# Optimization experiments

Measured on AMD Instinct MI355X. Metric: run time of the kernel, lower is better.

## Reference

```python
import jax, jax.numpy as jnp
import numpy as np

BIT = 8
Q_MAX = float(2 ** BIT - 1)  # 255
SMOOTH = 0.999


def hardsigmoid(x):
    # torch nn.Hardsigmoid: relu6(x + 3) / 6
    return jnp.clip(x / 6.0 + 0.5, 0.0, 1.0)


def setup_inputs() -> dict:
    key = jax.random.key(0)
    ks = jax.random.split(key, 5)
    B, C, H, W = 64, 256, 56, 56
    Cs = 64  # _make_divisible(256 // 4, 8)
    x = jax.random.normal(ks[0], (B, C, H, W), jnp.float32)
    w1 = jax.random.normal(ks[1], (Cs, C), jnp.float32) * 0.05  # fc1 1x1 conv weight
    b1 = jax.random.normal(ks[2], (Cs,), jnp.float32) * 0.05
    w2 = jax.random.normal(ks[3], (C, Cs), jnp.float32) * 0.05  # fc2 1x1 conv weight
    b2 = jax.random.normal(ks[4], (C,), jnp.float32) * 0.05
    act_range = jnp.array([-1.0, 1.0], jnp.float32)  # EMA-tracked (min, max) buffer
    return {"x": x, "w1": w1, "b1": b1, "w2": w2, "b2": b2, "act_range": act_range}


def reference(x, w1, b1, w2, b2, act_range):
    # squeeze: adaptive_avg_pool2d(input, 1) -> [B, C]
    pooled = jnp.mean(x, axis=(2, 3))
    # fc1: 1x1 conv + bias + ReLU
    h = jax.nn.relu(jnp.einsum('bc,sc->bs', pooled, w1) + b1)
    # fc2: 1x1 conv + bias, then quantized Hardsigmoid gate
    g = hardsigmoid(jnp.einsum('bs,cs->bc', h, w2) + b2)
    out = x * g[:, :, None, None]
    # training path: EMA min/max update + fake quantization (STE)
    rmin = jnp.min(out)
    rmax = jnp.max(out)
    new_min = act_range[0] * SMOOTH + rmin * (1.0 - SMOOTH)
    new_max = act_range[1] * SMOOTH + rmax * (1.0 - SMOOTH)
    s = (new_max - new_min) / Q_MAX
    z = -jnp.round(new_min / s)
    s = jax.lax.stop_gradient(s)
    z = jax.lax.stop_gradient(z)
    q = (jnp.clip(jnp.round(out / s + z), 0.0, Q_MAX) - z) * s
    # straight-through estimator
    return out + jax.lax.stop_gradient(q - out)
```

## Files before the change

### kernel.cpp

```cpp
#include <hip/hip_runtime.h>

#define B_   64
#define C_   256
#define BC   (B_ * C_)
#define CS   64
#define HW   3136
#define HW4  784
#define HW4F 768
#define HW4T 16

typedef float floatx4 __attribute__((ext_vector_type(4)));

__device__ __forceinline__ float fmin4(float4 v) {
    return fminf(fminf(v.x, v.y), fminf(v.z, v.w));
}
__device__ __forceinline__ float fmax4(float4 v) {
    return fmaxf(fmaxf(v.x, v.y), fmaxf(v.z, v.w));
}

__global__ __launch_bounds__(256) void k_pool(const float* __restrict__ x,
                                              float* __restrict__ pooled,
                                              float* __restrict__ xmn,
                                              float* __restrict__ xmx) {
    const int wave = threadIdx.x >> 6, lane = threadIdx.x & 63;
    const int bc = blockIdx.x * 4 + wave;
    const float4* xp = (const float4*)(x + (size_t)bc * HW);

    float sum = 0.0f;
    float mn = 3.402823466e38f;
    float mx = -3.402823466e38f;
    #pragma unroll
    for (int k = 0; k < 12; ++k) {
        float4 v = xp[lane + k * 64];
        sum += (v.x + v.y) + (v.z + v.w);
        mn = fminf(mn, fmin4(v));
        mx = fmaxf(mx, fmax4(v));
    }
    if (lane < HW4T) {
        float4 v = xp[HW4F + lane];
        sum += (v.x + v.y) + (v.z + v.w);
        mn = fminf(mn, fmin4(v));
        mx = fmaxf(mx, fmax4(v));
    }
    for (int off = 32; off > 0; off >>= 1) {
        sum += __shfl_down(sum, off, 64);
        mn = fminf(mn, __shfl_down(mn, off, 64));
        mx = fmaxf(mx, __shfl_down(mx, off, 64));
    }
    if (lane == 0) {
        pooled[bc] = sum / (float)HW;
        xmn[bc] = mn;
        xmx[bc] = mx;
    }
}

__global__ __launch_bounds__(256) void k_mid(const float* __restrict__ pooled,
                                             const float* __restrict__ w1,
                                             const float* __restrict__ b1,
                                             const float* __restrict__ w2,
                                             const float* __restrict__ b2,
                                             const float* __restrict__ xmn,
                                             const float* __restrict__ xmx,
                                             float* __restrict__ g,
                                             float* __restrict__ pmn,
                                             float* __restrict__ pmx) {
    const int b = blockIdx.x;
    const int t = threadIdx.x;
    __shared__ __align__(16) float p[C_];
    __shared__ __align__(16) float part[4][CS];
    __shared__ __align__(16) float hs[CS];
    p[t] = pooled[b * C_ + t];
    __syncthreads();

    {
        const int s_ = t & 63, q = t >> 6;
        const float4* wr = (const float4*)(w1 + s_ * C_ + q * 64);
        const float4* pr = (const float4*)(p + q * 64);
        float acc = 0.0f;
        #pragma unroll
        for (int k = 0; k < 16; ++k) {
            float4 w = wr[k], pv = pr[k];
            acc += w.x * pv.x + w.y * pv.y + w.z * pv.z + w.w * pv.w;
        }
        part[q][s_] = acc;
    }
    __syncthreads();
    if (t < CS) {
        float a = (part[0][t] + part[1][t]) + (part[2][t] + part[3][t]) + b1[t];
        hs[t] = fmaxf(a, 0.0f);
    }
    __syncthreads();

    float acc = b2[t];
    const float4* wr = (const float4*)(w2 + t * CS);
    const float4* hr = (const float4*)hs;
    #pragma unroll
    for (int k = 0; k < 16; ++k) {
        float4 w = wr[k], hv = hr[k];
        acc += w.x * hv.x + w.y * hv.y + w.z * hv.z + w.w * hv.w;
    }
    float gg = fminf(fmaxf(acc / 6.0f + 0.5f, 0.0f), 1.0f);
    const int i = b * C_ + t;
    g[i] = gg;
    float mn = gg * xmn[i];
    float mx = gg * xmx[i];
    for (int off = 32; off > 0; off >>= 1) {
        mn = fminf(mn, __shfl_down(mn, off, 64));
        mx = fmaxf(mx, __shfl_down(mx, off, 64));
    }
    __shared__ float smn[4], smx[4];
    const int wave = t >> 6, lane = t & 63;
    if (lane == 0) { smn[wave] = mn; smx[wave] = mx; }
    __syncthreads();
    if (t == 0) {
        pmn[b] = fminf(fminf(smn[0], smn[1]), fminf(smn[2], smn[3]));
        pmx[b] = fmaxf(fmaxf(smx[0], smx[1]), fmaxf(smx[2], smx[3]));
    }
}

__device__ __forceinline__ float quant1(float o, float s, float z, float inv_s) {
    float q = rintf(__builtin_fmaf(o, inv_s, z));
    q = fminf(fmaxf(q, 0.0f), 255.0f);
    return (q - z) * s;
}

__global__ __launch_bounds__(256) void k_quant(const float* __restrict__ x,
                                               const float* __restrict__ g,
                                               const float* __restrict__ pmn,
                                               const float* __restrict__ pmx,
                                               const float* __restrict__ act_range,
                                               float* __restrict__ out) {
    const int wave = threadIdx.x >> 6, lane = threadIdx.x & 63;

    float mn = pmn[lane];
    float mx = pmx[lane];
    for (int off = 32; off > 0; off >>= 1) {
        mn = fminf(mn, __shfl_xor(mn, off, 64));
        mx = fmaxf(mx, __shfl_xor(mx, off, 64));
    }
    const float new_min = act_range[0] * 0.999f + mn * 0.001f;
    const float new_max = act_range[1] * 0.999f + mx * 0.001f;
    const float s = (new_max - new_min) / 255.0f;
    const float z = -rintf(new_min / s);
    const float inv_s = 1.0f / s;

    const int bc = blockIdx.x * 4 + wave;
    const float gv = g[bc];
    const float4* xp = (const float4*)(x + (size_t)bc * HW);
    floatx4* op = (floatx4*)(out + (size_t)bc * HW);

    #pragma unroll
    for (int k = 0; k < 12; ++k) {
        const int i = lane + k * 64;
        float4 v = xp[i];
        floatx4 r;
        r.x = quant1(v.x * gv, s, z, inv_s);
        r.y = quant1(v.y * gv, s, z, inv_s);
        r.z = quant1(v.z * gv, s, z, inv_s);
        r.w = quant1(v.w * gv, s, z, inv_s);
        __builtin_nontemporal_store(r, op + i);
    }
    if (lane < HW4T) {
        const int i = HW4F + lane;
        float4 v = xp[i];
        floatx4 r;
        r.x = quant1(v.x * gv, s, z, inv_s);
        r.y = quant1(v.y * gv, s, z, inv_s);
        r.z = quant1(v.z * gv, s, z, inv_s);
        r.w = quant1(v.w * gv, s, z, inv_s);
        __builtin_nontemporal_store(r, op + i);
    }
}

extern "C" void kernel_launch(void* const* d_in, const int* in_sizes, int n_in,
                              void* d_out, int out_size, void* d_ws, size_t ws_size,
                              hipStream_t stream) {
    const float* x         = (const float*)d_in[0];
    const float* w1        = (const float*)d_in[1];
    const float* b1        = (const float*)d_in[2];
    const float* w2        = (const float*)d_in[3];
    const float* b2        = (const float*)d_in[4];
    const float* act_range = (const float*)d_in[5];
    float* out = (float*)d_out;

    float* ws     = (float*)d_ws;
    float* pooled = ws;
    float* xmn    = ws + BC;
    float* xmx    = ws + 2 * BC;
    float* g      = ws + 3 * BC;
    float* pmn    = ws + 4 * BC;
    float* pmx    = pmn + B_;

    k_pool <<<BC / 4, 256, 0, stream>>>(x, pooled, xmn, xmx);
    k_mid  <<<B_,     256, 0, stream>>>(pooled, w1, b1, w2, b2, xmn, xmx, g, pmn, pmx);
    k_quant<<<BC / 4, 256, 0, stream>>>(x, g, pmn, pmx, act_range, out);
}
```

Baseline: 384.3 us.

## Fuse pool, MLP and quantize stages into one cooperative persistent kernel

Replaces three separate kernel launches with a single cooperative persistent kernel that runs the pooling/minmax pass, the per-batch MLP gate, and the quantize pass, separated by grid-wide syncs. The aim is to remove launch gaps and tail idle time between stages. The cost is two grid barriers. The MLP stage also runs on only 64 of the blocks while the rest wait, and the grid is capped by occupancy at up to 2048 blocks. If the cooperative launch fails, it falls back to the old three-kernel path.

Result: slower. 611.9 us (+59.2%).

```diff
diff --git a/kernel.cpp b/kernel.cpp
--- a/kernel.cpp
+++ b/kernel.cpp
@@ -1,4 +1,7 @@
 #include <hip/hip_runtime.h>
+#include <hip/hip_cooperative_groups.h>
+
+namespace cg = cooperative_groups;
 
 #define B_   64
 #define C_   256
@@ -18,6 +21,154 @@
     return fmaxf(fmaxf(v.x, v.y), fmaxf(v.z, v.w));
 }
 
+__device__ __forceinline__ float quant1(float o, float s, float z, float inv_s) {
+    float q = rintf(__builtin_fmaf(o, inv_s, z));
+    q = fminf(fmaxf(q, 0.0f), 255.0f);
+    return (q - z) * s;
+}
+
+__global__ __launch_bounds__(256, 4) void k_fused(
+    const float* __restrict__ x,
+    const float* __restrict__ w1, const float* __restrict__ b1,
+    const float* __restrict__ w2, const float* __restrict__ b2,
+    const float* __restrict__ act_range,
+    float* __restrict__ out,
+    float* __restrict__ pooled, float* __restrict__ xmn, float* __restrict__ xmx,
+    float* __restrict__ g, float* __restrict__ pmn, float* __restrict__ pmx)
+{
+    cg::grid_group grid = cg::this_grid();
+    const int t = threadIdx.x;
+    const int wave = t >> 6, lane = t & 63;
+    const int gwave = blockIdx.x * 4 + wave;
+    const int nwave = gridDim.x * 4;
+
+    for (int bc = gwave; bc < BC; bc += nwave) {
+        const float4* xp = (const float4*)(x + (size_t)bc * HW);
+        float sum = 0.0f;
+        float mn = 3.402823466e38f;
+        float mx = -3.402823466e38f;
+        #pragma unroll
+        for (int k = 0; k < 12; ++k) {
+            float4 v = xp[lane + k * 64];
+            sum += (v.x + v.y) + (v.z + v.w);
+            mn = fminf(mn, fmin4(v));
+            mx = fmaxf(mx, fmax4(v));
+        }
+        if (lane < HW4T) {
+            float4 v = xp[HW4F + lane];
+            sum += (v.x + v.y) + (v.z + v.w);
+            mn = fminf(mn, fmin4(v));
+            mx = fmaxf(mx, fmax4(v));
+        }
+        for (int off = 32; off > 0; off >>= 1) {
+            sum += __shfl_down(sum, off, 64);
+            mn = fminf(mn, __shfl_down(mn, off, 64));
+            mx = fmaxf(mx, __shfl_down(mx, off, 64));
+        }
+        if (lane == 0) {
+            pooled[bc] = sum / (float)HW;
+            xmn[bc] = mn;
+            xmx[bc] = mx;
+        }
+    }
+    __threadfence();
+    grid.sync();
+
+    __shared__ __align__(16) float p[C_];
+    __shared__ __align__(16) float part[4][CS];
+    __shared__ __align__(16) float hs[CS];
+    __shared__ float smn[4], smx[4];
+    for (int b = blockIdx.x; b < B_; b += gridDim.x) {
+        p[t] = pooled[b * C_ + t];
+        __syncthreads();
+        {
+            const int s_ = t & 63, q = t >> 6;
+            const float4* wr = (const float4*)(w1 + s_ * C_ + q * 64);
+            const float4* pr = (const float4*)(p + q * 64);
+            float acc = 0.0f;
+            #pragma unroll
+            for (int k = 0; k < 16; ++k) {
+                float4 w = wr[k], pv = pr[k];
+                acc += w.x * pv.x + w.y * pv.y + w.z * pv.z + w.w * pv.w;
+            }
+            part[q][s_] = acc;
+        }
+        __syncthreads();
+        if (t < CS) {
+            float a = (part[0][t] + part[1][t]) + (part[2][t] + part[3][t]) + b1[t];
+            hs[t] = fmaxf(a, 0.0f);
+        }
+        __syncthreads();
+        float acc = b2[t];
+        const float4* wr = (const float4*)(w2 + t * CS);
+        const float4* hr = (const float4*)hs;
+        #pragma unroll
+        for (int k = 0; k < 16; ++k) {
+            float4 w = wr[k], hv = hr[k];
+            acc += w.x * hv.x + w.y * hv.y + w.z * hv.z + w.w * hv.w;
+        }
+        float gg = fminf(fmaxf(acc / 6.0f + 0.5f, 0.0f), 1.0f);
+        const int i = b * C_ + t;
+        g[i] = gg;
+        float mn = gg * xmn[i];
+        float mx = gg * xmx[i];
+        for (int off = 32; off > 0; off >>= 1) {
+            mn = fminf(mn, __shfl_down(mn, off, 64));
+            mx = fmaxf(mx, __shfl_down(mx, off, 64));
+        }
+        if (lane == 0) { smn[wave] = mn; smx[wave] = mx; }
+        __syncthreads();
+        if (t == 0) {
+            pmn[b] = fminf(fminf(smn[0], smn[1]), fminf(smn[2], smn[3]));
+            pmx[b] = fmaxf(fmaxf(smx[0], smx[1]), fmaxf(smx[2], smx[3]));
+        }
+        __syncthreads();
+    }
+    __threadfence();
+    grid.sync();
+
+    {
+        float mn = pmn[lane];
+        float mx = pmx[lane];
+        for (int off = 32; off > 0; off >>= 1) {
+            mn = fminf(mn, __shfl_xor(mn, off, 64));
+            mx = fmaxf(mx, __shfl_xor(mx, off, 64));
+        }
+        const float new_min = act_range[0] * 0.999f + mn * 0.001f;
+        const float new_max = act_range[1] * 0.999f + mx * 0.001f;
+        const float s = (new_max - new_min) / 255.0f;
+        const float z = -rintf(new_min / s);
+        const float inv_s = 1.0f / s;
+
+        for (int bc = gwave; bc < BC; bc += nwave) {
+            const float gv = g[bc];
+            const float4* xp = (const float4*)(x + (size_t)bc * HW);
+            floatx4* op = (floatx4*)(out + (size_t)bc * HW);
+            #pragma unroll
+            for (int k = 0; k < 12; ++k) {
+                const int i = lane + k * 64;
+                float4 v = xp[i];
+                floatx4 r;
+                r.x = quant1(v.x * gv, s, z, inv_s);
+                r.y = quant1(v.y * gv, s, z, inv_s);
+                r.z = quant1(v.z * gv, s, z, inv_s);
+                r.w = quant1(v.w * gv, s, z, inv_s);
+                __builtin_nontemporal_store(r, op + i);
+            }
+            if (lane < HW4T) {
+                const int i = HW4F + lane;
+                float4 v = xp[i];
+                floatx4 r;
+                r.x = quant1(v.x * gv, s, z, inv_s);
+                r.y = quant1(v.y * gv, s, z, inv_s);
+                r.z = quant1(v.z * gv, s, z, inv_s);
+                r.w = quant1(v.w * gv, s, z, inv_s);
+                __builtin_nontemporal_store(r, op + i);
+            }
+        }
+    }
+}
+
 __global__ __launch_bounds__(256) void k_pool(const float* __restrict__ x,
                                               float* __restrict__ pooled,
                                               float* __restrict__ xmn,
@@ -25,10 +176,8 @@
     const int wave = threadIdx.x >> 6, lane = threadIdx.x & 63;
     const int bc = blockIdx.x * 4 + wave;
     const float4* xp = (const float4*)(x + (size_t)bc * HW);
-
     float sum = 0.0f;
-    float mn = 3.402823466e38f;
-    float mx = -3.402823466e38f;
+    float mn = 3.402823466e38f, mx = -3.402823466e38f;
     #pragma unroll
     for (int k = 0; k < 12; ++k) {
         float4 v = xp[lane + k * 64];
@@ -71,7 +220,6 @@
     __shared__ __align__(16) float hs[CS];
     p[t] = pooled[b * C_ + t];
     __syncthreads();
-
     {
         const int s_ = t & 63, q = t >> 6;
         const float4* wr = (const float4*)(w1 + s_ * C_ + q * 64);
@@ -90,7 +238,6 @@
         hs[t] = fmaxf(a, 0.0f);
     }
     __syncthreads();
-
     float acc = b2[t];
     const float4* wr = (const float4*)(w2 + t * CS);
     const float4* hr = (const float4*)hs;
@@ -118,12 +265,6 @@
     }
 }
 
-__device__ __forceinline__ float quant1(float o, float s, float z, float inv_s) {
-    float q = rintf(__builtin_fmaf(o, inv_s, z));
-    q = fminf(fmaxf(q, 0.0f), 255.0f);
-    return (q - z) * s;
-}
-
 __global__ __launch_bounds__(256) void k_quant(const float* __restrict__ x,
                                                const float* __restrict__ g,
                                                const float* __restrict__ pmn,
@@ -131,7 +272,6 @@
                                                const float* __restrict__ act_range,
                                                float* __restrict__ out) {
     const int wave = threadIdx.x >> 6, lane = threadIdx.x & 63;
-
     float mn = pmn[lane];
     float mx = pmx[lane];
     for (int off = 32; off > 0; off >>= 1) {
@@ -148,7 +288,6 @@
     const float gv = g[bc];
     const float4* xp = (const float4*)(x + (size_t)bc * HW);
     floatx4* op = (floatx4*)(out + (size_t)bc * HW);
-
     #pragma unroll
     for (int k = 0; k < 12; ++k) {
         const int i = lane + k * 64;
@@ -191,7 +330,24 @@
     float* pmn    = ws + 4 * BC;
     float* pmx    = pmn + B_;
 
-    k_pool <<<BC / 4, 256, 0, stream>>>(x, pooled, xmn, xmx);
-    k_mid  <<<B_,     256, 0, stream>>>(pooled, w1, b1, w2, b2, xmn, xmx, g, pmn, pmx);
-    k_quant<<<BC / 4, 256, 0, stream>>>(x, g, pmn, pmx, act_range, out);
-}
+    static int nblk = 0;
+    if (nblk == 0) {
+        int perCU = 0;
+        hipError_t e = hipOccupancyMaxActiveBlocksPerMultiprocessor(&perCU, k_fused, 256, 0);
+        if (e != hipSuccess || perCU < 1) perCU = 4;
+        nblk = perCU * 256;
+        if (nblk > 2048) nblk = 2048;
+    }
+
+    void* args[] = {(void*)&x, (void*)&w1, (void*)&b1, (void*)&w2, (void*)&b2,
+                    (void*)&act_range, (void*)&out,
+                    (void*)&pooled, (void*)&xmn, (void*)&xmx,
+                    (void*)&g, (void*)&pmn, (void*)&pmx};
+    hipError_t err = hipLaunchCooperativeKernel((void*)k_fused, dim3(nblk), dim3(256),
+                                                args, 0, stream);
+    if (err != hipSuccess) {
+        k_pool <<<BC / 4, 256, 0, stream>>>(x, pooled, xmn, xmx);
+        k_mid  <<<B_,     256, 0, stream>>>(pooled, w1, b1, w2, b2, xmn, xmx, g, pmn, pmx);
+        k_quant<<<BC / 4, 256, 0, stream>>>(x, g, pmn, pmx, act_range, out);
+    }
+}
```
